# Kernel optimization log

Hardware: AMD Instinct MI355X
Metric: run time of the kernel (lower is better)

The kernel has to match this reference:

```python
import jax, jax.numpy as jnp
import numpy as np
from jax import lax


def setup_inputs() -> dict:
    key = jax.random.key(0)
    k1, k2, k3 = jax.random.split(key, 3)
    B, T, D, K = 64, 512, 1024, 32
    x = jax.random.normal(k1, (B, T, D), dtype=jnp.float32)
    W = jax.random.normal(k2, (D, K), dtype=jnp.float32) * (1.0 / np.sqrt(D))
    U = jax.random.normal(k3, (K, K), dtype=jnp.float32) * 0.1
    b = jnp.zeros((K,), dtype=jnp.float32)
    return {"x": x, "W": W, "U": U, "b": b}


def _crf_marginals(x, W, U, b):
    # Emission (input) energies: linear activation of x @ W + b -> [B, T, K]
    e = jnp.einsum('btd,dk->btk', x, W) + b
    e_t = jnp.swapaxes(e, 0, 1)  # [T, B, K]

    # Forward recursion: alpha_t = logsumexp_prev(alpha_{t-1} + U) + e_t
    def fwd_step(alpha, et):
        a = jax.nn.logsumexp(alpha[:, :, None] + U[None, :, :], axis=1) + et
        return a, a

    alpha0 = e_t[0]
    _, alphas = lax.scan(fwd_step, alpha0, e_t[1:])
    alpha = jnp.concatenate([alpha0[None], alphas], axis=0)  # [T, B, K]

    # Backward recursion: beta_t = logsumexp_next(U + e_{t+1} + beta_{t+1})
    def bwd_step(beta, et_next):
        nb = jax.nn.logsumexp(U[None, :, :] + (et_next + beta)[:, None, :], axis=2)
        return nb, nb

    betaT = jnp.zeros_like(alpha0)
    _, betas = lax.scan(bwd_step, betaT, e_t[1:], reverse=True)
    beta = jnp.concatenate([betas, betaT[None]], axis=0)  # [T, B, K]

    # Marginal probability of each tag at each timestep
    marg = jax.nn.softmax(alpha + beta, axis=-1)  # [T, B, K]
    return jnp.swapaxes(marg, 0, 1)  # [B, T, K]


def reference(x, W, U, b):
    return _crf_marginals(x, W, U, b)
```

## Files before the change

kernel.cpp:

```cpp
#include <hip/hip_runtime.h>
#include <stdint.h>

#define TT 512
#define BB 64
#define DD 1024
#define KK 32

__device__ __forceinline__ float rfl(float v) {
  return __int_as_float(__builtin_amdgcn_readfirstlane(__float_as_int(v)));
}

__device__ __forceinline__ void gload_lds16(const float4* g, float4* l) {
  __builtin_amdgcn_global_load_lds(
      (const __attribute__((address_space(1))) uint32_t*)g,
      (__attribute__((address_space(3))) uint32_t*)l, 16, 0, 0);
}

__global__ __launch_bounds__(256, 8) void emit_kernel(
    const float* __restrict__ x, const float* __restrict__ W,
    const float* __restrict__ bias, float* __restrict__ F) {
  __shared__ float4 Ls4[1024];
  const int t = threadIdx.x;
  const int l = t & 63;
  const int w = t >> 6;
  const int rg = l >> 2;
  const int kg = l & 3;
  const int m0 = blockIdx.x * 16;
  const int r = m0 + rg;

  const float* xp = x + (size_t)r * DD + w * 256;

  float acc[8];
#pragma unroll
  for (int k = 0; k < 8; ++k) acc[k] = 0.f;

  float4 xa = *(const float4*)(xp);

  const float4* Wg4 = (const float4*)(W) + (size_t)w * 2048;
  float4* Lw = &Ls4[w * 256];

#pragma unroll 1
  for (int c = 0; c < 8; ++c) {
#pragma unroll
    for (int i = 0; i < 4; ++i)
      gload_lds16(Wg4 + c * 256 + i * 64 + l, Lw + i * 64);
    asm volatile("s_waitcnt vmcnt(0)" ::: "memory");

#pragma unroll
    for (int gg = 0; gg < 8; ++gg) {
      const int dd = c * 32 + gg * 4;
      int nd = dd + 4; if (nd > 252) nd = 252;
      float4 xb = *(const float4*)(xp + nd);
#pragma unroll
      for (int d2 = 0; d2 < 4; ++d2) {
        const int wb = w * 256 + (gg * 4 + d2) * 8 + kg * 2;
        float4 wlo = Ls4[wb];
        float4 whi = Ls4[wb + 1];
        const float x0 = ((const float*)&xa)[d2];
        acc[0] = fmaf(x0, wlo.x, acc[0]); acc[1] = fmaf(x0, wlo.y, acc[1]);
        acc[2] = fmaf(x0, wlo.z, acc[2]); acc[3] = fmaf(x0, wlo.w, acc[3]);
        acc[4] = fmaf(x0, whi.x, acc[4]); acc[5] = fmaf(x0, whi.y, acc[5]);
        acc[6] = fmaf(x0, whi.z, acc[6]); acc[7] = fmaf(x0, whi.w, acc[7]);
      }
      xa = xb;
    }
  }

  __syncthreads();
  Ls4[w * 128 + rg * 8 + kg * 2] =
      make_float4(acc[0], acc[1], acc[2], acc[3]);
  Ls4[w * 128 + rg * 8 + kg * 2 + 1] =
      make_float4(acc[4], acc[5], acc[6], acc[7]);
  __syncthreads();
  if (t < 128) {
    const int rr = t >> 3;
    const int kc = t & 7;
    float4 s = Ls4[rr * 8 + kc];
#pragma unroll
    for (int q = 1; q < 4; ++q) {
      float4 a = Ls4[q * 128 + rr * 8 + kc];
      s.x += a.x; s.y += a.y; s.z += a.z; s.w += a.w;
    }
    float4 bv = *(const float4*)(bias + kc * 4);
    float4 e;
    e.x = __expf(s.x + bv.x); e.y = __expf(s.y + bv.y);
    e.z = __expf(s.z + bv.z); e.w = __expf(s.w + bv.w);
    ((float4*)(F + (size_t)(m0 + rr) * KK))[kc] = e;
  }
}

__global__ __launch_bounds__(64) void scan_kernel(
    const float* __restrict__ F, const float* __restrict__ U,
    float* __restrict__ A, float* __restrict__ Bw) {
  __shared__ __align__(16) float cur[KK];
  const int l = threadIdx.x;
  const int kk = l & 31;
  const int h = l >> 5;
  const int seg = blockIdx.x & 15;
  const int b = (blockIdx.x >> 4) & 63;
  const int dir = blockIdx.x >> 10;

  const float* Fb = F + (size_t)b * TT * KK;
  float V[16];

  if (dir == 0) {
    float* Ab = A + (size_t)b * TT * KK;
#pragma unroll
    for (int j = 0; j < 16; ++j) V[j] = __expf(U[(h * 16 + j) * KK + kk]);
    const int lo = seg * 32, hi = seg * 32 + 31;
    const int t0 = (seg == 0) ? 0 : lo - 17;
    float a = Fb[t0 * KK + kk];
    cur[kk] = a;
    if (seg == 0 && l < 32) Ab[l] = a;
    __builtin_amdgcn_wave_barrier();

#define FSTEP(fv, tcur)                                                     \
    {                                                                       \
      const float4* c4 = (const float4*)cur;                                \
      float4 y0 = c4[h*4+0], y1 = c4[h*4+1], y2 = c4[h*4+2], y3 = c4[h*4+3];\
      float r = __builtin_amdgcn_rcpf(rfl(y0.x));                           \
      float s0 = fmaf(y0.x, V[0],  fmaf(y0.y, V[1],                         \
                 fmaf(y0.z, V[2],  y0.w * V[3])));                          \
      float s1 = fmaf(y1.x, V[4],  fmaf(y1.y, V[5],                         \
                 fmaf(y1.z, V[6],  y1.w * V[7])));                          \
      float s2 = fmaf(y2.x, V[8],  fmaf(y2.y, V[9],                         \
                 fmaf(y2.z, V[10], y2.w * V[11])));                         \
      float s3 = fmaf(y3.x, V[12], fmaf(y3.y, V[13],                        \
                 fmaf(y3.z, V[14], y3.w * V[15])));                         \
      float s = (s0 + s1) + (s2 + s3);                                      \
      s += __shfl_xor(s, 32);                                               \
      a = s * ((fv) * r);                                                   \
      cur[kk] = a;                                                          \
      __builtin_amdgcn_wave_barrier();                                      \
      if ((tcur) >= lo && l < 32) Ab[(tcur) * KK + l] = a;                  \
    }

    int t = t0 + 1;
    float f0 = Fb[t * KK + kk],       f1 = Fb[(t + 1) * KK + kk];
    float f2 = Fb[(t + 2) * KK + kk], f3 = Fb[(t + 3) * KK + kk];
    for (; t + 3 <= hi; t += 4) {
      int tn = t + 4;
      int u0 = tn     > hi ? hi : tn;
      int u1 = tn + 1 > hi ? hi : tn + 1;
      int u2 = tn + 2 > hi ? hi : tn + 2;
      int u3 = tn + 3 > hi ? hi : tn + 3;
      float n0 = Fb[u0 * KK + kk], n1 = Fb[u1 * KK + kk];
      float n2 = Fb[u2 * KK + kk], n3 = Fb[u3 * KK + kk];
      FSTEP(f0, t); FSTEP(f1, t + 1); FSTEP(f2, t + 2); FSTEP(f3, t + 3);
      f0 = n0; f1 = n1; f2 = n2; f3 = n3;
    }
    if (t <= hi) { FSTEP(f0, t); ++t; }
    if (t <= hi) { FSTEP(f1, t); ++t; }
    if (t <= hi) { FSTEP(f2, t); ++t; }
#undef FSTEP
  } else {
    const int b2 = b;
    float* Bb = Bw + (size_t)b2 * TT * KK;
#pragma unroll
    for (int j = 0; j < 16; ++j) V[j] = __expf(U[kk * KK + h * 16 + j]);
    const int lo = seg * 32;
    const int hs = seg * 32 + 31;
    const int t1 = (seg == 15) ? (TT - 1) : (lo + 48);
    float g = Fb[t1 * KK + kk];
    cur[kk] = g;
    if (seg == 15 && l < 32) Bb[(TT - 1) * KK + l] = 1.0f;
    __builtin_amdgcn_wave_barrier();

#define BSTEP(fv, tcur)                                                     \
    {                                                                       \
      const float4* c4 = (const float4*)cur;                                \
      float4 y0 = c4[h*4+0], y1 = c4[h*4+1], y2 = c4[h*4+2], y3 = c4[h*4+3];\
      float r = __builtin_amdgcn_rcpf(rfl(y0.x));                           \
      float s0 = fmaf(y0.x, V[0],  fmaf(y0.y, V[1],                         \
                 fmaf(y0.z, V[2],  y0.w * V[3])));                          \
      float s1 = fmaf(y1.x, V[4],  fmaf(y1.y, V[5],                         \
                 fmaf(y1.z, V[6],  y1.w * V[7])));                          \
      float s2 = fmaf(y2.x, V[8],  fmaf(y2.y, V[9],                         \
                 fmaf(y2.z, V[10], y2.w * V[11])));                         \
      float s3 = fmaf(y3.x, V[12], fmaf(y3.y, V[13],                        \
                 fmaf(y3.z, V[14], y3.w * V[15])));                         \
      float s = (s0 + s1) + (s2 + s3);                                      \
      s += __shfl_xor(s, 32);                                               \
      float bnew = s * r;                                                   \
      g = bnew * (fv);                                                      \
      cur[kk] = g;                                                          \
      __builtin_amdgcn_wave_barrier();                                      \
      if ((tcur) <= hs && l < 32) Bb[(tcur) * KK + l] = bnew;               \
    }

    int t = t1 - 1;
    float f0 = Fb[t * KK + kk],       f1 = Fb[(t - 1) * KK + kk];
    float f2 = Fb[(t - 2) * KK + kk], f3 = Fb[(t - 3) * KK + kk];
    for (; t - 3 >= lo; t -= 4) {
      int tn = t - 4;
      int u0 = tn     < 0 ? 0 : tn;
      int u1 = tn - 1 < 0 ? 0 : tn - 1;
      int u2 = tn - 2 < 0 ? 0 : tn - 2;
      int u3 = tn - 3 < 0 ? 0 : tn - 3;
      float n0 = Fb[u0 * KK + kk], n1 = Fb[u1 * KK + kk];
      float n2 = Fb[u2 * KK + kk], n3 = Fb[u3 * KK + kk];
      BSTEP(f0, t); BSTEP(f1, t - 1); BSTEP(f2, t - 2); BSTEP(f3, t - 3);
      f0 = n0; f1 = n1; f2 = n2; f3 = n3;
    }
    if (t >= lo) { BSTEP(f0, t); --t; }
    if (t >= lo) { BSTEP(f1, t); --t; }
    if (t >= lo) { BSTEP(f2, t); --t; }
#undef BSTEP
  }
}

__global__ __launch_bounds__(256) void combine_kernel(
    const float* __restrict__ Bw, float* __restrict__ out) {
  size_t i = (size_t)blockIdx.x * 256 + threadIdx.x;
  float p = out[i] * Bw[i];
  float ssum = p;
  ssum += __shfl_xor(ssum, 1);
  ssum += __shfl_xor(ssum, 2);
  ssum += __shfl_xor(ssum, 4);
  ssum += __shfl_xor(ssum, 8);
  ssum += __shfl_xor(ssum, 16);
  out[i] = p / ssum;
}

extern "C" void kernel_launch(void* const* d_in, const int* in_sizes, int n_in,
                              void* d_out, int out_size, void* d_ws, size_t ws_size,
                              hipStream_t stream) {
  const float* x = (const float*)d_in[0];
  const float* W = (const float*)d_in[1];
  const float* U = (const float*)d_in[2];
  const float* b = (const float*)d_in[3];
  float* out = (float*)d_out;
  float* F = (float*)d_ws;
  float* Bw = F + (size_t)BB * TT * KK;

  emit_kernel<<<2048, 256, 0, stream>>>(x, W, b, F);
  scan_kernel<<<2048, 64, 0, stream>>>(F, U, out, Bw);
  combine_kernel<<<(BB * TT * KK) / 256, 256, 0, stream>>>(Bw, out);
}
```

Measured before the change: 237.8 us.

## Compute two rows per thread in emission GEMM with 8-way D split

Each thread now accumulates two rows of x against the same W values read from LDS, halving LDS traffic per FMA. The reduction dimension is split across eight waves in 512-thread blocks covering 32 rows, and the cross-wave reduction grows to eight partials. In exchange the kernel uses more registers and LDS, and there are half as many blocks, which may lower occupancy. The emission pass is memory bound on reading x, so the benefit may be limited.

```diff
diff --git a/kernel.cpp b/kernel.cpp
--- a/kernel.cpp
+++ b/kernel.cpp
@@ -16,31 +16,35 @@
       (__attribute__((address_space(3))) uint32_t*)l, 16, 0, 0);
 }
 
-__global__ __launch_bounds__(256, 8) void emit_kernel(
+__global__ __launch_bounds__(512, 8) void emit_kernel(
     const float* __restrict__ x, const float* __restrict__ W,
     const float* __restrict__ bias, float* __restrict__ F) {
-  __shared__ float4 Ls4[1024];
+  __shared__ float4 Ls4[2048];
   const int t = threadIdx.x;
   const int l = t & 63;
   const int w = t >> 6;
   const int rg = l >> 2;
   const int kg = l & 3;
-  const int m0 = blockIdx.x * 16;
-  const int r = m0 + rg;
-
-  const float* xp = x + (size_t)r * DD + w * 256;
-
-  float acc[8];
-#pragma unroll
-  for (int k = 0; k < 8; ++k) acc[k] = 0.f;
-
-  float4 xa = *(const float4*)(xp);
-
-  const float4* Wg4 = (const float4*)(W) + (size_t)w * 2048;
+  const int m0 = blockIdx.x * 32;
+  const int r0 = m0 + rg * 2;
+
+  const float* xp0 = x + (size_t)r0 * DD + w * 128;
+  const float* xp1 = xp0 + DD;
+
+  float acc[2][8];
+#pragma unroll
+  for (int j = 0; j < 2; ++j)
+#pragma unroll
+    for (int k = 0; k < 8; ++k) acc[j][k] = 0.f;
+
+  float4 xa0 = *(const float4*)(xp0);
+  float4 xa1 = *(const float4*)(xp1);
+
+  const float4* Wg4 = (const float4*)(W) + (size_t)w * 1024;
   float4* Lw = &Ls4[w * 256];
 
 #pragma unroll 1
-  for (int c = 0; c < 8; ++c) {
+  for (int c = 0; c < 4; ++c) {
 #pragma unroll
     for (int i = 0; i < 4; ++i)
       gload_lds16(Wg4 + c * 256 + i * 64 + l, Lw + i * 64);
@@ -48,37 +52,46 @@
 
 #pragma unroll
     for (int gg = 0; gg < 8; ++gg) {
-      const int dd = c * 32 + gg * 4;
-      int nd = dd + 4; if (nd > 252) nd = 252;
-      float4 xb = *(const float4*)(xp + nd);
+      const int dl = c * 32 + gg * 4;
+      int nd = dl + 4; if (nd > 124) nd = 124;
+      float4 xb0 = *(const float4*)(xp0 + nd);
+      float4 xb1 = *(const float4*)(xp1 + nd);
 #pragma unroll
       for (int d2 = 0; d2 < 4; ++d2) {
         const int wb = w * 256 + (gg * 4 + d2) * 8 + kg * 2;
         float4 wlo = Ls4[wb];
         float4 whi = Ls4[wb + 1];
-        const float x0 = ((const float*)&xa)[d2];
-        acc[0] = fmaf(x0, wlo.x, acc[0]); acc[1] = fmaf(x0, wlo.y, acc[1]);
-        acc[2] = fmaf(x0, wlo.z, acc[2]); acc[3] = fmaf(x0, wlo.w, acc[3]);
-        acc[4] = fmaf(x0, whi.x, acc[4]); acc[5] = fmaf(x0, whi.y, acc[5]);
-        acc[6] = fmaf(x0, whi.z, acc[6]); acc[7] = fmaf(x0, whi.w, acc[7]);
+        const float x0 = ((const float*)&xa0)[d2];
+        const float x1 = ((const float*)&xa1)[d2];
+        acc[0][0]=fmaf(x0,wlo.x,acc[0][0]); acc[0][1]=fmaf(x0,wlo.y,acc[0][1]);
+        acc[0][2]=fmaf(x0,wlo.z,acc[0][2]); acc[0][3]=fmaf(x0,wlo.w,acc[0][3]);
+        acc[0][4]=fmaf(x0,whi.x,acc[0][4]); acc[0][5]=fmaf(x0,whi.y,acc[0][5]);
+        acc[0][6]=fmaf(x0,whi.z,acc[0][6]); acc[0][7]=fmaf(x0,whi.w,acc[0][7]);
+        acc[1][0]=fmaf(x1,wlo.x,acc[1][0]); acc[1][1]=fmaf(x1,wlo.y,acc[1][1]);
+        acc[1][2]=fmaf(x1,wlo.z,acc[1][2]); acc[1][3]=fmaf(x1,wlo.w,acc[1][3]);
+        acc[1][4]=fmaf(x1,whi.x,acc[1][4]); acc[1][5]=fmaf(x1,whi.y,acc[1][5]);
+        acc[1][6]=fmaf(x1,whi.z,acc[1][6]); acc[1][7]=fmaf(x1,whi.w,acc[1][7]);
       }
-      xa = xb;
+      xa0 = xb0; xa1 = xb1;
     }
   }
 
   __syncthreads();
-  Ls4[w * 128 + rg * 8 + kg * 2] =
-      make_float4(acc[0], acc[1], acc[2], acc[3]);
-  Ls4[w * 128 + rg * 8 + kg * 2 + 1] =
-      make_float4(acc[4], acc[5], acc[6], acc[7]);
+#pragma unroll
+  for (int j = 0; j < 2; ++j) {
+    Ls4[w * 256 + (rg * 2 + j) * 8 + kg * 2] =
+        make_float4(acc[j][0], acc[j][1], acc[j][2], acc[j][3]);
+    Ls4[w * 256 + (rg * 2 + j) * 8 + kg * 2 + 1] =
+        make_float4(acc[j][4], acc[j][5], acc[j][6], acc[j][7]);
+  }
   __syncthreads();
-  if (t < 128) {
+  if (t < 256) {
     const int rr = t >> 3;
     const int kc = t & 7;
     float4 s = Ls4[rr * 8 + kc];
 #pragma unroll
-    for (int q = 1; q < 4; ++q) {
-      float4 a = Ls4[q * 128 + rr * 8 + kc];
+    for (int q = 1; q < 8; ++q) {
+      float4 a = Ls4[q * 256 + rr * 8 + kc];
       s.x += a.x; s.y += a.y; s.z += a.z; s.w += a.w;
     }
     float4 bv = *(const float4*)(bias + kc * 4);
@@ -233,7 +246,7 @@
   float* F = (float*)d_ws;
   float* Bw = F + (size_t)BB * TT * KK;
 
-  emit_kernel<<<2048, 256, 0, stream>>>(x, W, b, F);
+  emit_kernel<<<1024, 512, 0, stream>>>(x, W, b, F);
   scan_kernel<<<2048, 64, 0, stream>>>(F, U, out, Bw);
   combine_kernel<<<(BB * TT * KK) / 256, 256, 0, stream>>>(Bw, out);
 }
```

After: 240.0 us. Within noise of the previous version (+0.9%).

## Retile emission GEMM to 64 rows per block with double-buffered LDS staging

Applied to the files above, without the earlier changes.

The emission GEMM now processes 64 rows per block instead of 16, so each W tile loaded into LDS is reused across four times as many rows. x tiles are also staged through LDS with an XOR swizzle to avoid bank conflicts. A two-stage double buffer with partial vmcnt waits overlaps global-to-LDS loads with FMA work. The cost is more LDS per block (48KB), more accumulator registers, lower occupancy (launch bounds 4) and a quarter as many blocks.

```diff
diff --git a/kernel.cpp b/kernel.cpp
--- a/kernel.cpp
+++ b/kernel.cpp
@@ -16,69 +16,108 @@
       (__attribute__((address_space(3))) uint32_t*)l, 16, 0, 0);
 }
 
-__global__ __launch_bounds__(256, 8) void emit_kernel(
+__global__ __launch_bounds__(256, 4) void emit_kernel(
     const float* __restrict__ x, const float* __restrict__ W,
     const float* __restrict__ bias, float* __restrict__ F) {
-  __shared__ float4 Ls4[1024];
+  __shared__ float4 Ls4[3072];
   const int t = threadIdx.x;
   const int l = t & 63;
   const int w = t >> 6;
   const int rg = l >> 2;
   const int kg = l & 3;
-  const int m0 = blockIdx.x * 16;
-  const int r = m0 + rg;
-
-  const float* xp = x + (size_t)r * DD + w * 256;
-
-  float acc[8];
-#pragma unroll
-  for (int k = 0; k < 8; ++k) acc[k] = 0.f;
-
-  float4 xa = *(const float4*)(xp);
-
-  const float4* Wg4 = (const float4*)(W) + (size_t)w * 2048;
-  float4* Lw = &Ls4[w * 256];
+  const int m0 = blockIdx.x * 64;
+
+  const int wb4 = w * 768;
+  float4* Lw = &Ls4[wb4];
+  float4* Lx = &Ls4[wb4 + 256];
+
+  const float* Wlane = W + (size_t)(w * 256 + (l >> 3)) * KK + (l & 7) * 4;
+  const float* Xlane = x + (size_t)(m0 + (l >> 2)) * DD + w * 256
+                         + 4 * ((l & 3) ^ ((l >> 4) & 3));
+
+#define STAGE(c, p) do {                                                    \
+    const float* ws_ = Wlane + (size_t)(c) * 16 * KK;                       \
+    gload_lds16((const float4*)(ws_),           Lw + (p) * 128);            \
+    gload_lds16((const float4*)(ws_ + 8 * KK),  Lw + (p) * 128 + 64);       \
+    const float* xs_ = Xlane + (c) * 16;                                    \
+    gload_lds16((const float4*)(xs_),               Lx + (p) * 256);        \
+    gload_lds16((const float4*)(xs_ + 16 * DD),     Lx + (p) * 256 + 64);   \
+    gload_lds16((const float4*)(xs_ + 32 * DD),     Lx + (p) * 256 + 128);  \
+    gload_lds16((const float4*)(xs_ + 48 * DD),     Lx + (p) * 256 + 192);  \
+  } while (0)
+
+#define COMPUTE(p) do {                                                     \
+    const float4* Wb = Lw + (p) * 128;                                      \
+    const float4* Xb = Lx + (p) * 256;                                      \
+    _Pragma("unroll")                                                       \
+    for (int gg = 0; gg < 4; ++gg) {                                        \
+      const int xsw = gg ^ (rg & 3);             \
+      float4 xr[4];                                                         \
+      _Pragma("unroll")                                                     \
+      for (int j = 0; j < 4; ++j) xr[j] = Xb[(4 * rg + j) * 4 + xsw];       \
+      _Pragma("unroll")                                                     \
+      for (int dd = 0; dd < 4; ++dd) {                                      \
+        float4 wlo = Wb[(gg * 4 + dd) * 8 + kg * 2];                        \
+        float4 whi = Wb[(gg * 4 + dd) * 8 + kg * 2 + 1];                    \
+        _Pragma("unroll")                                                   \
+        for (int j = 0; j < 4; ++j) {                                       \
+          const float xv = ((const float*)&xr[j])[dd];                      \
+          acc[j][0] = fmaf(xv, wlo.x, acc[j][0]);                           \
+          acc[j][1] = fmaf(xv, wlo.y, acc[j][1]);                           \
+          acc[j][2] = fmaf(xv, wlo.z, acc[j][2]);                           \
+          acc[j][3] = fmaf(xv, wlo.w, acc[j][3]);                           \
+          acc[j][4] = fmaf(xv, whi.x, acc[j][4]);                           \
+          acc[j][5] = fmaf(xv, whi.y, acc[j][5]);                           \
+          acc[j][6] = fmaf(xv, whi.z, acc[j][6]);                           \
+          acc[j][7] = fmaf(xv, whi.w, acc[j][7]);                           \
+        }                                                                   \
+      }                                                                     \
+    }                                                                       \
+  } while (0)
+
+  float acc[4][8];
+#pragma unroll
+  for (int j = 0; j < 4; ++j)
+#pragma unroll
+    for (int k = 0; k < 8; ++k) acc[j][k] = 0.f;
+
+  STAGE(0, 0);
+  STAGE(1, 1);
 
 #pragma unroll 1
-  for (int c = 0; c < 8; ++c) {
-#pragma unroll
-    for (int i = 0; i < 4; ++i)
-      gload_lds16(Wg4 + c * 256 + i * 64 + l, Lw + i * 64);
-    asm volatile("s_waitcnt vmcnt(0)" ::: "memory");
-
-#pragma unroll
-    for (int gg = 0; gg < 8; ++gg) {
-      const int dd = c * 32 + gg * 4;
-      int nd = dd + 4; if (nd > 252) nd = 252;
-      float4 xb = *(const float4*)(xp + nd);
-#pragma unroll
-      for (int d2 = 0; d2 < 4; ++d2) {
-        const int wb = w * 256 + (gg * 4 + d2) * 8 + kg * 2;
-        float4 wlo = Ls4[wb];
-        float4 whi = Ls4[wb + 1];
-        const float x0 = ((const float*)&xa)[d2];
-        acc[0] = fmaf(x0, wlo.x, acc[0]); acc[1] = fmaf(x0, wlo.y, acc[1]);
-        acc[2] = fmaf(x0, wlo.z, acc[2]); acc[3] = fmaf(x0, wlo.w, acc[3]);
-        acc[4] = fmaf(x0, whi.x, acc[4]); acc[5] = fmaf(x0, whi.y, acc[5]);
-        acc[6] = fmaf(x0, whi.z, acc[6]); acc[7] = fmaf(x0, whi.w, acc[7]);
-      }
-      xa = xb;
-    }
-  }
+  for (int c = 0; c < 14; ++c) {
+    const int p = c & 1;
+    asm volatile("s_waitcnt vmcnt(6)" ::: "memory");
+    COMPUTE(p);
+    asm volatile("" ::: "memory");
+    STAGE(c + 2, p);
+  }
+  asm volatile("s_waitcnt vmcnt(6)" ::: "memory");
+  COMPUTE(0);
+  asm volatile("s_waitcnt vmcnt(0)" ::: "memory");
+  COMPUTE(1);
+
+#undef STAGE
+#undef COMPUTE
 
   __syncthreads();
-  Ls4[w * 128 + rg * 8 + kg * 2] =
-      make_float4(acc[0], acc[1], acc[2], acc[3]);
-  Ls4[w * 128 + rg * 8 + kg * 2 + 1] =
-      make_float4(acc[4], acc[5], acc[6], acc[7]);
+#pragma unroll
+  for (int j = 0; j < 4; ++j) {
+    Ls4[wb4 + (4 * rg + j) * 8 + kg * 2] =
+        make_float4(acc[j][0], acc[j][1], acc[j][2], acc[j][3]);
+    Ls4[wb4 + (4 * rg + j) * 8 + kg * 2 + 1] =
+        make_float4(acc[j][4], acc[j][5], acc[j][6], acc[j][7]);
+  }
   __syncthreads();
-  if (t < 128) {
-    const int rr = t >> 3;
-    const int kc = t & 7;
-    float4 s = Ls4[rr * 8 + kc];
+#pragma unroll
+  for (int rep = 0; rep < 2; ++rep) {
+    const int idx = t + rep * 256;
+    const int rr = idx >> 3;
+    const int kc = idx & 7;
+    float4 s = Ls4[idx];
 #pragma unroll
     for (int q = 1; q < 4; ++q) {
-      float4 a = Ls4[q * 128 + rr * 8 + kc];
+      float4 a = Ls4[q * 768 + idx];
       s.x += a.x; s.y += a.y; s.z += a.z; s.w += a.w;
     }
     float4 bv = *(const float4*)(bias + kc * 4);
@@ -233,7 +272,7 @@
   float* F = (float*)d_ws;
   float* Bw = F + (size_t)BB * TT * KK;
 
-  emit_kernel<<<2048, 256, 0, stream>>>(x, W, b, F);
+  emit_kernel<<<512, 256, 0, stream>>>(x, W, b, F);
   scan_kernel<<<2048, 64, 0, stream>>>(F, U, out, Bw);
   combine_kernel<<<(BB * TT * KK) / 256, 256, 0, stream>>>(Bw, out);
 }
```

New measurement: 219.6 us. 7.7% less time.

## Retile emission GEMM to 128-row blocks with double-buffered LDS staging

Applied to the files above, without the earlier changes.

Reworks the x@W emission kernel so each block handles 128 rows instead of 16, with each thread holding an 8x8 register accumulator tile. Both x and W chunks are streamed into LDS through async global_load_lds in a two-stage pipeline, with an XOR swizzle on the x tile to avoid bank conflicts. The goal is more reuse of W per load and overlap of memory loads with FMA work. In exchange the grid shrinks from 2048 to 256 blocks, register pressure rises, and occupancy drops.

```diff
diff --git a/kernel.cpp b/kernel.cpp
--- a/kernel.cpp
+++ b/kernel.cpp
@@ -16,76 +16,133 @@
       (__attribute__((address_space(3))) uint32_t*)l, 16, 0, 0);
 }
 
-__global__ __launch_bounds__(256, 8) void emit_kernel(
+__global__ __launch_bounds__(256) void emit_kernel(
     const float* __restrict__ x, const float* __restrict__ W,
     const float* __restrict__ bias, float* __restrict__ F) {
-  __shared__ float4 Ls4[1024];
+  __shared__ float4 Ls4[2560];
   const int t = threadIdx.x;
   const int l = t & 63;
-  const int w = t >> 6;
+  const int q = t >> 6;
   const int rg = l >> 2;
   const int kg = l & 3;
-  const int m0 = blockIdx.x * 16;
-  const int r = m0 + rg;
-
-  const float* xp = x + (size_t)r * DD + w * 256;
-
-  float acc[8];
-#pragma unroll
-  for (int k = 0; k < 8; ++k) acc[k] = 0.f;
-
-  float4 xa = *(const float4*)(xp);
-
-  const float4* Wg4 = (const float4*)(W) + (size_t)w * 2048;
-  float4* Lw = &Ls4[w * 256];
+  const int m0 = blockIdx.x * 128;
+
+  float4* Lx = &Ls4[q * 640];
+  float4* Lw = &Ls4[q * 640 + 512];
+
+  const float* Wlane = W + (size_t)(q * 256 + (l >> 3)) * KK + (l & 7) * 4;
+  const float* Xl0; const float* Xl1; const float* Xl2; const float* Xl3;
+  {
+    const int base_q = q * 256;
+#define XSRC(i)                                                              \
+    ({ int s_ = (i) * 64 + l; int rgs_ = s_ >> 4;                            \
+       int v_ = (s_ & 15) ^ (rgs_ & 7);                                      \
+       x + (size_t)(m0 + rgs_ * 8 + (v_ >> 1)) * DD + base_q + (v_ & 1) * 4; })
+    Xl0 = XSRC(0); Xl1 = XSRC(1); Xl2 = XSRC(2); Xl3 = XSRC(3);
+#undef XSRC
+  }
+
+#define STAGE(c, p) do {                                                     \
+    gload_lds16((const float4*)(Wlane + (size_t)(c) * 256), Lw + (p) * 64);  \
+    gload_lds16((const float4*)(Xl0 + (c) * 8), Lx + (p) * 256);             \
+    gload_lds16((const float4*)(Xl1 + (c) * 8), Lx + (p) * 256 + 64);        \
+    gload_lds16((const float4*)(Xl2 + (c) * 8), Lx + (p) * 256 + 128);       \
+    gload_lds16((const float4*)(Xl3 + (c) * 8), Lx + (p) * 256 + 192);       \
+  } while (0)
+
+#define COMPUTE(p) do {                                                      \
+    const float4* Xb = Lx + (p) * 256;                                       \
+    const float4* Wb = Lw + (p) * 64;                                        \
+    _Pragma("unroll")                                                        \
+    for (int hf = 0; hf < 2; ++hf) {                                         \
+      float4 xr[8];                                                          \
+      _Pragma("unroll")                                                      \
+      for (int j = 0; j < 8; ++j)                                            \
+        xr[j] = Xb[rg * 16 + ((j * 2 + hf) ^ (rg & 7))];                     \
+      _Pragma("unroll")                                                      \
+      for (int d2 = 0; d2 < 4; ++d2) {                                       \
+        const int dd = hf * 4 + d2;                                          \
+        float4 wlo = Wb[dd * 8 + kg * 2];                                    \
+        float4 whi = Wb[dd * 8 + kg * 2 + 1];                                \
+        _Pragma("unroll")                                                    \
+        for (int j = 0; j < 8; ++j) {                                        \
+          const float xv = ((const float*)&xr[j])[d2];                       \
+          acc[j][0] = fmaf(xv, wlo.x, acc[j][0]);                            \
+          acc[j][1] = fmaf(xv, wlo.y, acc[j][1]);                            \
+          acc[j][2] = fmaf(xv, wlo.z, acc[j][2]);                            \
+          acc[j][3] = fmaf(xv, wlo.w, acc[j][3]);                            \
+          acc[j][4] = fmaf(xv, whi.x, acc[j][4]);                            \
+          acc[j][5] = fmaf(xv, whi.y, acc[j][5]);                            \
+          acc[j][6] = fmaf(xv, whi.z, acc[j][6]);                            \
+          acc[j][7] = fmaf(xv, whi.w, acc[j][7]);                            \
+        }                                                                    \
+      }                                                                      \
+    }                                                                        \
+  } while (0)
+
+  float acc[8][8];
+#pragma unroll
+  for (int j = 0; j < 8; ++j)
+#pragma unroll
+    for (int k = 0; k < 8; ++k) acc[j][k] = 0.f;
+
+  STAGE(0, 0);
+  STAGE(1, 1);
 
 #pragma unroll 1
-  for (int c = 0; c < 8; ++c) {
-#pragma unroll
-    for (int i = 0; i < 4; ++i)
-      gload_lds16(Wg4 + c * 256 + i * 64 + l, Lw + i * 64);
-    asm volatile("s_waitcnt vmcnt(0)" ::: "memory");
-
-#pragma unroll
-    for (int gg = 0; gg < 8; ++gg) {
-      const int dd = c * 32 + gg * 4;
-      int nd = dd + 4; if (nd > 252) nd = 252;
-      float4 xb = *(const float4*)(xp + nd);
-#pragma unroll
-      for (int d2 = 0; d2 < 4; ++d2) {
-        const int wb = w * 256 + (gg * 4 + d2) * 8 + kg * 2;
-        float4 wlo = Ls4[wb];
-        float4 whi = Ls4[wb + 1];
-        const float x0 = ((const float*)&xa)[d2];
-        acc[0] = fmaf(x0, wlo.x, acc[0]); acc[1] = fmaf(x0, wlo.y, acc[1]);
-        acc[2] = fmaf(x0, wlo.z, acc[2]); acc[3] = fmaf(x0, wlo.w, acc[3]);
-        acc[4] = fmaf(x0, whi.x, acc[4]); acc[5] = fmaf(x0, whi.y, acc[5]);
-        acc[6] = fmaf(x0, whi.z, acc[6]); acc[7] = fmaf(x0, whi.w, acc[7]);
+  for (int c = 0; c < 30; ++c) {
+    const int p = c & 1;
+    asm volatile("s_waitcnt vmcnt(5)" ::: "memory");
+    COMPUTE(p);
+    asm volatile("" ::: "memory");
+    STAGE(c + 2, p);
+  }
+  asm volatile("s_waitcnt vmcnt(5)" ::: "memory");
+  COMPUTE(0);
+  asm volatile("s_waitcnt vmcnt(0)" ::: "memory");
+  COMPUTE(1);
+
+#undef STAGE
+#undef COMPUTE
+
+  __syncthreads();
+#pragma unroll 1
+  for (int half = 0; half < 2; ++half) {
+    if ((rg >> 3) == half) {
+      const int rl = (rg & 7) * 8;
+#pragma unroll
+      for (int j = 0; j < 8; ++j) {
+        Ls4[q * 512 + (rl + j) * 8 + kg * 2] =
+            make_float4(acc[j][0], acc[j][1], acc[j][2], acc[j][3]);
+        Ls4[q * 512 + (rl + j) * 8 + kg * 2 + 1] =
+            make_float4(acc[j][4], acc[j][5], acc[j][6], acc[j][7]);
       }
-      xa = xb;
-    }
-  }
-
-  __syncthreads();
-  Ls4[w * 128 + rg * 8 + kg * 2] =
-      make_float4(acc[0], acc[1], acc[2], acc[3]);
-  Ls4[w * 128 + rg * 8 + kg * 2 + 1] =
-      make_float4(acc[4], acc[5], acc[6], acc[7]);
-  __syncthreads();
-  if (t < 128) {
-    const int rr = t >> 3;
-    const int kc = t & 7;
-    float4 s = Ls4[rr * 8 + kc];
-#pragma unroll
-    for (int q = 1; q < 4; ++q) {
-      float4 a = Ls4[q * 128 + rr * 8 + kc];
-      s.x += a.x; s.y += a.y; s.z += a.z; s.w += a.w;
-    }
-    float4 bv = *(const float4*)(bias + kc * 4);
-    float4 e;
-    e.x = __expf(s.x + bv.x); e.y = __expf(s.y + bv.y);
-    e.z = __expf(s.z + bv.z); e.w = __expf(s.w + bv.w);
-    ((float4*)(F + (size_t)(m0 + rr) * KK))[kc] = e;
+    }
+    __syncthreads();
+    {
+      const int rr = t >> 2;
+      const int kf = (t & 3) * 2;
+      float4 s0 = Ls4[rr * 8 + kf];
+      float4 s1 = Ls4[rr * 8 + kf + 1];
+#pragma unroll
+      for (int qq = 1; qq < 4; ++qq) {
+        float4 a0 = Ls4[qq * 512 + rr * 8 + kf];
+        float4 a1 = Ls4[qq * 512 + rr * 8 + kf + 1];
+        s0.x += a0.x; s0.y += a0.y; s0.z += a0.z; s0.w += a0.w;
+        s1.x += a1.x; s1.y += a1.y; s1.z += a1.z; s1.w += a1.w;
+      }
+      float4 bb0 = *(const float4*)(bias + kf * 4);
+      float4 bb1 = *(const float4*)(bias + kf * 4 + 4);
+      float4 e0, e1;
+      e0.x = __expf(s0.x + bb0.x); e0.y = __expf(s0.y + bb0.y);
+      e0.z = __expf(s0.z + bb0.z); e0.w = __expf(s0.w + bb0.w);
+      e1.x = __expf(s1.x + bb1.x); e1.y = __expf(s1.y + bb1.y);
+      e1.z = __expf(s1.z + bb1.z); e1.w = __expf(s1.w + bb1.w);
+      float4* F4 = (float4*)(F + (size_t)(m0 + half * 64 + rr) * KK);
+      F4[kf] = e0;
+      F4[kf + 1] = e1;
+    }
+    __syncthreads();
   }
 }
 
@@ -233,7 +290,7 @@
   float* F = (float*)d_ws;
   float* Bw = F + (size_t)BB * TT * KK;
 
-  emit_kernel<<<2048, 256, 0, stream>>>(x, W, b, F);
+  emit_kernel<<<256, 256, 0, stream>>>(x, W, b, F);
   scan_kernel<<<2048, 64, 0, stream>>>(F, U, out, Bw);
   combine_kernel<<<(BB * TT * KK) / 256, 256, 0, stream>>>(Bw, out);
 }
```

New measurement: 235.6 us. About the same (-1.0%).
